# Kernel optimization log

Measured on AMD Instinct MI355X. Metric: run time of the kernel, lower is better.

## Reference

```python
import jax, jax.numpy as jnp
from jax import lax
import numpy as np

T, I, H, H2 = 2048, 64, 256, 1024  # time steps, input feats, hidden, hidden2


def _lstm(x, Wih, Whh, bih, bhh):
    """PyTorch-convention LSTM. x: [T, B, I]; Wih: [4H, I]; Whh: [4H, H].
    Gate order i, f, g, o. Returns hidden states [T, B, H]."""
    Hd = Whh.shape[1]
    b = bih + bhh
    xw = jnp.einsum('tbi,gi->tbg', x, Wih) + b  # precompute input projections

    def step(carry, xt):
        h, c = carry
        z = xt + h @ Whh.T
        i, f, g, o = jnp.split(z, 4, axis=-1)
        c = jax.nn.sigmoid(f) * c + jax.nn.sigmoid(i) * jnp.tanh(g)
        h = jax.nn.sigmoid(o) * jnp.tanh(c)
        return (h, c), h

    h0 = jnp.zeros((x.shape[1], Hd), x.dtype)
    _, hs = lax.scan(step, (h0, h0), xw)
    return hs


def setup_inputs() -> dict:
    key = jax.random.key(0)
    ks = jax.random.split(key, 16)
    s1 = 1.0 / np.sqrt(H)
    s2 = 1.0 / np.sqrt(H2)
    d = {
        'x': jax.random.normal(ks[0], (T, I, 21), jnp.float32),
        'Wih1': jax.random.uniform(ks[1], (4 * H, I), jnp.float32, -s1, s1),
        'Whh1': jax.random.uniform(ks[2], (4 * H, H), jnp.float32, -s1, s1),
        'bih1': jax.random.uniform(ks[3], (4 * H,), jnp.float32, -s1, s1),
        'bhh1': jax.random.uniform(ks[4], (4 * H,), jnp.float32, -s1, s1),
        'Wih2': jax.random.uniform(ks[5], (4 * H2, H * 21), jnp.float32, -s2, s2),
        'Whh2': jax.random.uniform(ks[6], (4 * H2, H2), jnp.float32, -s2, s2),
        'bih2': jax.random.uniform(ks[7], (4 * H2,), jnp.float32, -s2, s2),
        'bhh2': jax.random.uniform(ks[8], (4 * H2,), jnp.float32, -s2, s2),
        'Wih3': jax.random.uniform(ks[9], (4 * H, H2), jnp.float32, -s1, s1),
        'Whh3': jax.random.uniform(ks[10], (4 * H, H), jnp.float32, -s1, s1),
        'bih3': jax.random.uniform(ks[11], (4 * H,), jnp.float32, -s1, s1),
        'bhh3': jax.random.uniform(ks[12], (4 * H,), jnp.float32, -s1, s1),
        'Wfc': jax.random.uniform(ks[13], (21, H), jnp.float32, -s1, s1),
        'bfc': jax.random.uniform(ks[14], (21,), jnp.float32, -s1, s1),
    }
    return d


def reference(x, Wih1, Whh1, bih1, bhh1, Wih2, Whh2, bih2, bhh2,
              Wih3, Whh3, bih3, bhh3, Wfc, bfc):
    # The 21-iteration torch loop runs lstm1 independently on each of the 21
    # channel slices with batch=1; fold the 21 channels into the batch dim.
    x1 = jnp.transpose(x, (0, 2, 1))           # [T, 21, I]
    h1 = _lstm(x1, Wih1, Whh1, bih1, bhh1)     # [T, 21, H]
    # x_torch[:, :, i*H:(i+1)*H] = channel i -> channel-major concat
    xcat = h1.reshape(T, 1, 21 * H)            # [T, 1, 21H]
    h2 = _lstm(xcat, Wih2, Whh2, bih2, bhh2)   # [T, 1, H2]
    h3 = _lstm(h2, Wih3, Whh3, bih3, bhh3)     # [T, 1, H]
    out = h3 @ Wfc.T + bfc                     # [T, 1, 21]
    return out
```

## Files before the change

### kernel.cpp

```cpp
#include <hip/hip_runtime.h>


#define T_STEPS 2048
#define SENT 0xFFFFFFFFu

using f4v   = __attribute__((ext_vector_type(4))) float;
using s8v   = __attribute__((ext_vector_type(8))) short;
using u16x8 = __attribute__((ext_vector_type(8))) unsigned short;
using u32x4 = __attribute__((ext_vector_type(4))) unsigned;

__device__ __forceinline__ unsigned short f2bf(float v) {
  unsigned u = __float_as_uint(v);
  u = (u + 0x7FFFu + ((u >> 16) & 1u)) >> 16;
  return (unsigned short)u;
}
__device__ __forceinline__ float bf2f(unsigned short b) {
  return __uint_as_float(((unsigned)b) << 16);
}
__device__ __forceinline__ unsigned packhl(float v) {
  unsigned short hb = f2bf(v);
  unsigned short lb = f2bf(v - bf2f(hb));
  return (((unsigned)hb) << 16) | lb;
}
__device__ __forceinline__ float unpackhl(unsigned p) {
  return __uint_as_float(p & 0xFFFF0000u) + __uint_as_float(p << 16);
}
__device__ __forceinline__ float sigm(float x) { return 1.0f / (1.0f + __expf(-x)); }
__device__ __forceinline__ float tanh_f(float x) {
  float ax = fabsf(x);
  float e = __expf(-2.0f * ax);
  float t = (1.0f - e) / (1.0f + e);
  return copysignf(t, x);
}
__device__ __forceinline__ unsigned ld_agent32(const unsigned* p) {
  return __hip_atomic_load(p, __ATOMIC_RELAXED, __HIP_MEMORY_SCOPE_AGENT);
}
__device__ __forceinline__ void st_agent32(unsigned* p, unsigned v) {
  __hip_atomic_store(p, v, __ATOMIC_RELAXED, __HIP_MEMORY_SCOPE_AGENT);
}
__device__ __forceinline__ void ctr_add(unsigned* p) {
  __hip_atomic_fetch_add(p, 1u, __ATOMIC_RELAXED, __HIP_MEMORY_SCOPE_AGENT);
}
__device__ __forceinline__ void poll_ctr(const unsigned* p, unsigned tgt) {
  unsigned n = 0;
  while (ld_agent32(p) < tgt) {
    if (++n > (1u << 22)) break;
    __builtin_amdgcn_s_sleep(4);
  }
}
__device__ __forceinline__ u32x4 ld16_coh(const unsigned* addr) {
  u32x4 c;
  asm volatile("global_load_dwordx4 %0, %1, off sc0 sc1\n\t"
               "s_waitcnt vmcnt(0)"
               : "=&v"(c) : "v"(addr) : "memory");
  return c;
}
#define VMCNT0() asm volatile("s_waitcnt vmcnt(0)" ::: "memory")

#define L16(M) M(0) M(1) M(2) M(3) M(4) M(5) M(6) M(7) M(8) M(9) M(10) M(11) \
  M(12) M(13) M(14) M(15)
#define L64(M) L16(M) M(16) M(17) M(18) M(19) M(20) M(21) M(22) M(23) M(24) \
  M(25) M(26) M(27) M(28) M(29) M(30) M(31) M(32) M(33) M(34) M(35) M(36) \
  M(37) M(38) M(39) M(40) M(41) M(42) M(43) M(44) M(45) M(46) M(47) M(48) \
  M(49) M(50) M(51) M(52) M(53) M(54) M(55) M(56) M(57) M(58) M(59) M(60) \
  M(61) M(62) M(63)

__device__ __forceinline__ void unpack8(u32x4 a, u32x4 b, u16x8& hi, u16x8& lo) {
#pragma unroll
  for (int j = 0; j < 4; ++j) {
    hi[j]     = (unsigned short)(a[j] >> 16);
    lo[j]     = (unsigned short)(a[j] & 0xFFFFu);
    hi[4 + j] = (unsigned short)(b[j] >> 16);
    lo[4 + j] = (unsigned short)(b[j] & 0xFFFFu);
  }
}

__device__ void gemm_tile_packed(
    const unsigned* __restrict__ Ap, const unsigned short* __restrict__ Bh,
    const unsigned short* __restrict__ Bl, const float* __restrict__ b1,
    const float* __restrict__ b2, unsigned* __restrict__ C,
    int tm, int tn, int K, int N, char* smem)
{
  unsigned short* lds = (unsigned short*)smem;
  const size_t m0 = (size_t)tm * 128, n0 = (size_t)tn * 128;
  const int tid = threadIdx.x, lane = tid & 63, w = tid >> 6;
  const int wr = w >> 1, wc = w & 1;
  const int srow = tid >> 2, sc8 = (tid & 3) * 8;

  const unsigned* pA = Ap + m0 * K;
  const unsigned short* pBh = Bh + n0 * K;
  const unsigned short* pBl = Bl + n0 * K;

  f4v acc[4][4];
#pragma unroll
  for (int i = 0; i < 4; ++i)
#pragma unroll
    for (int j = 0; j < 4; ++j) acc[i][j] = f4v{0.f, 0.f, 0.f, 0.f};

  u32x4 a00, a01, a10, a11;
  u16x8 s4, s5, s6, s7;
#define LOADK(k0)                                                           \
  a00 = *(const u32x4*)(pA + (size_t)srow * K + (k0) + sc8);                \
  a01 = *(const u32x4*)(pA + (size_t)srow * K + (k0) + sc8 + 4);            \
  a10 = *(const u32x4*)(pA + (size_t)(srow + 64) * K + (k0) + sc8);         \
  a11 = *(const u32x4*)(pA + (size_t)(srow + 64) * K + (k0) + sc8 + 4);     \
  s4 = *(const u16x8*)(pBh + (size_t)srow * K + (k0) + sc8);                \
  s5 = *(const u16x8*)(pBh + (size_t)(srow + 64) * K + (k0) + sc8);         \
  s6 = *(const u16x8*)(pBl + (size_t)srow * K + (k0) + sc8);                \
  s7 = *(const u16x8*)(pBl + (size_t)(srow + 64) * K + (k0) + sc8);

  LOADK(0);
  const int fr = lane & 15, fko = (lane >> 4) * 8;
  for (int k0 = 0; k0 < K; k0 += 32) {
    u16x8 h0, l0, h1, l1;
    unpack8(a00, a01, h0, l0);
    unpack8(a10, a11, h1, l1);
    *(u16x8*)&lds[0     +  srow       * 32 + sc8] = h0;
    *(u16x8*)&lds[0     + (srow + 64) * 32 + sc8] = h1;
    *(u16x8*)&lds[4096  +  srow       * 32 + sc8] = l0;
    *(u16x8*)&lds[4096  + (srow + 64) * 32 + sc8] = l1;
    *(u16x8*)&lds[8192  +  srow       * 32 + sc8] = s4;
    *(u16x8*)&lds[8192  + (srow + 64) * 32 + sc8] = s5;
    *(u16x8*)&lds[12288 +  srow       * 32 + sc8] = s6;
    *(u16x8*)&lds[12288 + (srow + 64) * 32 + sc8] = s7;
    __syncthreads();
    if (k0 + 32 < K) { LOADK(k0 + 32); }
    s8v afh[4], afl[4], bfh[4], bfl[4];
#pragma unroll
    for (int i = 0; i < 4; ++i) {
      int ar = (64 * wr + 16 * i + fr) * 32 + fko;
      int br = (64 * wc + 16 * i + fr) * 32 + fko;
      afh[i] = *(const s8v*)&lds[0 + ar];
      afl[i] = *(const s8v*)&lds[4096 + ar];
      bfh[i] = *(const s8v*)&lds[8192 + br];
      bfl[i] = *(const s8v*)&lds[12288 + br];
    }
#pragma unroll
    for (int mi = 0; mi < 4; ++mi)
#pragma unroll
      for (int ni = 0; ni < 4; ++ni) {
        acc[mi][ni] = __builtin_amdgcn_mfma_f32_16x16x32_bf16(afh[mi], bfh[ni], acc[mi][ni], 0, 0, 0);
        acc[mi][ni] = __builtin_amdgcn_mfma_f32_16x16x32_bf16(afh[mi], bfl[ni], acc[mi][ni], 0, 0, 0);
        acc[mi][ni] = __builtin_amdgcn_mfma_f32_16x16x32_bf16(afl[mi], bfh[ni], acc[mi][ni], 0, 0, 0);
      }
    __syncthreads();
  }
#undef LOADK
  const int er = (lane >> 4) * 4, ec = lane & 15;
#pragma unroll
  for (int ni = 0; ni < 4; ++ni) {
    size_t col = n0 + 64 * wc + 16 * ni + ec;
    float bv = b1[col] + b2[col];
#pragma unroll
    for (int mi = 0; mi < 4; ++mi) {
      size_t row = m0 + 64 * wr + 16 * mi + er;
#pragma unroll
      for (int rr = 0; rr < 4; ++rr)
        st_agent32(&C[(row + rr) * N + col], __float_as_uint(acc[mi][ni][rr] + bv));
    }
  }
}

__global__ __launch_bounds__(256, 1) void mega_kernel(
    const float* __restrict__ x,
    const float* __restrict__ Wih1, const float* __restrict__ Whh1,
    const float* __restrict__ bih1, const float* __restrict__ bhh1,
    const float* __restrict__ Whh2,
    const float* __restrict__ bih2, const float* __restrict__ bhh2,
    const float* __restrict__ Whh3,
    const float* __restrict__ bih3, const float* __restrict__ bhh3,
    unsigned* __restrict__ h1r0, unsigned* __restrict__ h2r0,
    unsigned* __restrict__ h3r0, unsigned* __restrict__ cnt,
    unsigned* __restrict__ h1rows, unsigned* __restrict__ h2rows,
    unsigned* __restrict__ h3rows,
    float* __restrict__ xw2, float* __restrict__ xw3,
    const unsigned short* __restrict__ wih2h, const unsigned short* __restrict__ wih2l,
    const unsigned short* __restrict__ wih3h, const unsigned short* __restrict__ wih3l)
{
  __shared__ __align__(16) char smem[32768];
  unsigned* ready1 = cnt + 0;
  unsigned* done2  = cnt + 16;
  unsigned* ready2 = cnt + 32;
  unsigned* done3  = cnt + 48;
  const int wg = blockIdx.x;
  const int widx = threadIdx.x >> 6, lane = threadIdx.x & 63;

  if (wg < 84) {
    const int c = wg / 4, sub = wg % 4;
    const int gwv = sub * 4 + widx;
    const int u16i = lane & 15, g = lane >> 4;
    const int grow = g * 256 + gwv * 16 + u16i;

    const f4v* wsrc = (const f4v*)(Whh1 + (size_t)grow * 256);
    const f4v* xsrc = (const f4v*)(Wih1 + (size_t)grow * 64);
#define DH(i) f4v m##i = wsrc[i];
#define DX(i) f4v n##i = xsrc[i];
    L64(DH)
    L16(DX)
#undef DH
#undef DX
    const float bias = bih1[grow] + bhh1[grow];

    float* const hb = (float*)smem + widx * 320;
    float* const xq = hb + 256;

    float cst = 0.0f;
    float xpre = x[(size_t)lane * 21 + c];

    for (int t = 0; t < T_STEPS; ++t) {
      xq[lane] = xpre;
      if (t + 1 < T_STEPS) xpre = x[(size_t)(t + 1) * 1344 + lane * 21 + c];
      const unsigned* src = t ? h1rows + (size_t)(t - 1) * 5376 + c * 256
                              : h1r0 + c * 256;
      const unsigned* addr = src + 4 * lane;
      u32x4 c0;
      unsigned n = 0;
      for (;;) {
        c0 = ld16_coh(addr);
        bool ok = (c0[0] != SENT) && (c0[1] != SENT) &&
                  (c0[2] != SENT) && (c0[3] != SENT);
        if (ok || ++n > (1u << 18)) break;
      }
      *(f4v*)&hb[4 * lane] = f4v{unpackhl(c0[0]), unpackhl(c0[1]),
                                 unpackhl(c0[2]), unpackhl(c0[3])};
      float a0 = 0, a1 = 0, a2 = 0, a3 = 0;
#define FH(i) { f4v h4 = *(const f4v*)&hb[4 * i]; \
  a0 = fmaf(m##i[0], h4[0], a0); a1 = fmaf(m##i[1], h4[1], a1); \
  a2 = fmaf(m##i[2], h4[2], a2); a3 = fmaf(m##i[3], h4[3], a3); }
#define FX(i) { f4v x4 = *(const f4v*)&xq[4 * i]; \
  a0 = fmaf(n##i[0], x4[0], a0); a1 = fmaf(n##i[1], x4[1], a1); \
  a2 = fmaf(n##i[2], x4[2], a2); a3 = fmaf(n##i[3], x4[3], a3); }
      L64(FH)
      L16(FX)
#undef FH
#undef FX
      float z = (a0 + a1) + (a2 + a3) + bias;
      float zi = __shfl(z, u16i);
      float zf = __shfl(z, 16 + u16i);
      float zg = __shfl(z, 32 + u16i);
      float zo = __shfl(z, 48 + u16i);
      if (lane < 16) {
        float cn = sigm(zf) * cst + sigm(zi) * tanh_f(zg);
        float hn = sigm(zo) * tanh_f(cn);
        cst = cn;
        st_agent32(&h1rows[(size_t)t * 5376 + c * 256 + gwv * 16 + lane], packhl(hn));
      }
      if ((t & 127) == 127) {
        VMCNT0();
        if (lane == 0) ctr_add(&ready1[t >> 7]);
      }
    }
  } else if (wg < 148) {
    const int gw = (wg - 84) * 4 + widx;
    const int q = lane >> 4, r4 = lane & 15;
    const int u = r4 & 3, g = r4 >> 2;
    const int grow = g * 1024 + gw * 4 + u;

    const f4v* wsrc = (const f4v*)(Whh2 + (size_t)grow * 1024 + q * 256);
#define DW(i) f4v w##i = wsrc[i];
    L64(DW)
#undef DW

    float* const wls = (float*)smem + widx * 1040;
    const float* const qreg = wls + q * 260;

    float cst = 0.0f;
    float xwn = 0.0f;

    for (int t = 0; t < T_STEPS; ++t) {
      float xwv;
      if ((t & 127) == 0) {
        poll_ctr(&done2[t >> 7], 32);
        xwv = xw2[(size_t)t * 4096 + grow];
      } else xwv = xwn;
      {
        const unsigned* src = t ? h2rows + (size_t)(t - 1) * 1024 : h2r0;
        const unsigned* addr = src + 4 * lane;
        u32x4 c0, c1, c2, c3;
        unsigned n = 0;
        for (;;) {
          asm volatile(
              "global_load_dwordx4 %0, %4, off sc0 sc1\n\t"
              "global_load_dwordx4 %1, %4, off offset:1024 sc0 sc1\n\t"
              "global_load_dwordx4 %2, %4, off offset:2048 sc0 sc1\n\t"
              "global_load_dwordx4 %3, %4, off offset:3072 sc0 sc1\n\t"
              "s_waitcnt vmcnt(0)"
              : "=&v"(c0), "=&v"(c1), "=&v"(c2), "=&v"(c3)
              : "v"(addr) : "memory");
          bool ok = true;
#pragma unroll
          for (int j = 0; j < 4; ++j)
            ok = ok && (c0[j] != SENT) && (c1[j] != SENT) &&
                       (c2[j] != SENT) && (c3[j] != SENT);
          if (ok || ++n > (1u << 18)) break;
        }
        *(f4v*)&wls[0 * 260 + 4 * lane] = f4v{unpackhl(c0[0]), unpackhl(c0[1]), unpackhl(c0[2]), unpackhl(c0[3])};
        *(f4v*)&wls[1 * 260 + 4 * lane] = f4v{unpackhl(c1[0]), unpackhl(c1[1]), unpackhl(c1[2]), unpackhl(c1[3])};
        *(f4v*)&wls[2 * 260 + 4 * lane] = f4v{unpackhl(c2[0]), unpackhl(c2[1]), unpackhl(c2[2]), unpackhl(c2[3])};
        *(f4v*)&wls[3 * 260 + 4 * lane] = f4v{unpackhl(c3[0]), unpackhl(c3[1]), unpackhl(c3[2]), unpackhl(c3[3])};
      }
      float a0 = 0, a1 = 0, a2 = 0, a3 = 0;
#define FW(i) { f4v h4 = *(const f4v*)&qreg[4 * i]; \
  a0 = fmaf(w##i[0], h4[0], a0); a1 = fmaf(w##i[1], h4[1], a1); \
  a2 = fmaf(w##i[2], h4[2], a2); a3 = fmaf(w##i[3], h4[3], a3); }
      L64(FW)
#undef FW
      float z = (a0 + a1) + (a2 + a3);
      z += __shfl_xor(z, 16);
      z += __shfl_xor(z, 32);
      z += xwv;
      float zi  = __shfl(z, u);
      float zf  = __shfl(z, 4 + u);
      float zg2 = __shfl(z, 8 + u);
      float zo  = __shfl(z, 12 + u);
      if (lane < 4) {
        float cn = sigm(zf) * cst + sigm(zi) * tanh_f(zg2);
        float hn = sigm(zo) * tanh_f(cn);
        cst = cn;
        st_agent32(&h2rows[(size_t)t * 1024 + gw * 4 + lane], packhl(hn));
      }
      if ((t & 127) == 127) {
        VMCNT0();
        if (lane == 0) ctr_add(&ready2[t >> 7]);
      }
      if (t + 1 < T_STEPS && ((t + 1) & 127) != 0)
        xwn = xw2[(size_t)(t + 1) * 4096 + grow];
    }
  } else if (wg < 152) {
    const int gw = (wg - 148) * 4 + widx;
    const int u16i = lane & 15, g = lane >> 4;
    const int grow = g * 256 + gw * 16 + u16i;

    const f4v* wsrc = (const f4v*)(Whh3 + (size_t)grow * 256);
#define DW(i) f4v w##i = wsrc[i];
    L64(DW)
#undef DW

    float* const hb = (float*)smem + widx * 256;
    float cst = 0.0f;
    float xwn = 0.0f;

    for (int t = 0; t < T_STEPS; ++t) {
      float xwv;
      if ((t & 127) == 0) {
        poll_ctr(&done3[t >> 7], 8);
        xwv = xw3[(size_t)t * 1024 + grow];
      } else xwv = xwn;
      const unsigned* src = t ? h3rows + (size_t)(t - 1) * 256 : h3r0;
      const unsigned* addr = src + 4 * lane;
      u32x4 c0;
      unsigned n = 0;
      for (;;) {
        c0 = ld16_coh(addr);
        bool ok = (c0[0] != SENT) && (c0[1] != SENT) &&
                  (c0[2] != SENT) && (c0[3] != SENT);
        if (ok || ++n > (1u << 18)) break;
      }
      *(f4v*)&hb[4 * lane] = f4v{__uint_as_float(c0[0]), __uint_as_float(c0[1]),
                                 __uint_as_float(c0[2]), __uint_as_float(c0[3])};
      float a0 = 0, a1 = 0, a2 = 0, a3 = 0;
#define FW(i) { f4v h4 = *(const f4v*)&hb[4 * i]; \
  a0 = fmaf(w##i[0], h4[0], a0); a1 = fmaf(w##i[1], h4[1], a1); \
  a2 = fmaf(w##i[2], h4[2], a2); a3 = fmaf(w##i[3], h4[3], a3); }
      L64(FW)
#undef FW
      float z = (a0 + a1) + (a2 + a3) + xwv;
      float zi = __shfl(z, u16i);
      float zf = __shfl(z, 16 + u16i);
      float zg = __shfl(z, 32 + u16i);
      float zo = __shfl(z, 48 + u16i);
      if (lane < 16) {
        float cn = sigm(zf) * cst + sigm(zi) * tanh_f(zg);
        float hn = sigm(zo) * tanh_f(cn);
        cst = cn;
        st_agent32(&h3rows[(size_t)t * 256 + gw * 16 + lane], __float_as_uint(hn));
      }
      if (t + 1 < T_STEPS && ((t + 1) & 127) != 0)
        xwn = xw3[(size_t)(t + 1) * 1024 + grow];
    }
  } else if (wg < 206) {
    const int pw = wg - 152;
    for (int i = pw; i < 512; i += 54) {
      int tm = i >> 5, tn = i & 31;
      poll_ctr(&ready1[tm], 336);
      gemm_tile_packed(h1rows, wih2h, wih2l, bih2, bhh2,
                       (unsigned*)xw2, tm, tn, 5376, 4096, smem);
      VMCNT0();
      __syncthreads();
      if (threadIdx.x == 0) ctr_add(&done2[tm]);
      __syncthreads();
    }
  } else {
    const int pw = wg - 206;
    for (int i = pw; i < 128; i += 14) {
      int tm = i >> 3, tn = i & 7;
      poll_ctr(&ready2[tm], 256);
      gemm_tile_packed(h2rows, wih3h, wih3l, bih3, bhh3,
                       (unsigned*)xw3, tm, tn, 1024, 1024, smem);
      VMCNT0();
      __syncthreads();
      if (threadIdx.x == 0) ctr_add(&done3[tm]);
      __syncthreads();
    }
  }
}

__global__ void split_kernel(const float* __restrict__ src,
                             unsigned short* __restrict__ hi,
                             unsigned short* __restrict__ lo, int n) {
  int i = blockIdx.x * 256 + threadIdx.x;
  if (i < n) {
    float v = src[i];
    unsigned short hb = f2bf(v);
    hi[i] = hb;
    lo[i] = f2bf(v - bf2f(hb));
  }
}

__global__ void fc_kernel(const float* __restrict__ h3, const float* __restrict__ Wfc,
                          const float* __restrict__ bfc, float* __restrict__ out) {
  int t = blockIdx.x, m = threadIdx.x;
  if (m < 21) {
    const float* hp = h3 + (size_t)t * 256;
    const float* wp = Wfc + m * 256;
    float a = 0.0f;
#pragma unroll 8
    for (int j = 0; j < 256; ++j) a = fmaf(wp[j], hp[j], a);
    out[t * 21 + m] = a + bfc[m];
  }
}

extern "C" void kernel_launch(void* const* d_in, const int* in_sizes, int n_in,
                              void* d_out, int out_size, void* d_ws, size_t ws_size,
                              hipStream_t stream) {
  const float* x    = (const float*)d_in[0];
  const float* Wih1 = (const float*)d_in[1];
  const float* Whh1 = (const float*)d_in[2];
  const float* bih1 = (const float*)d_in[3];
  const float* bhh1 = (const float*)d_in[4];
  const float* Wih2 = (const float*)d_in[5];
  const float* Whh2 = (const float*)d_in[6];
  const float* bih2 = (const float*)d_in[7];
  const float* bhh2 = (const float*)d_in[8];
  const float* Wih3 = (const float*)d_in[9];
  const float* Whh3 = (const float*)d_in[10];
  const float* bih3 = (const float*)d_in[11];
  const float* bhh3 = (const float*)d_in[12];
  const float* Wfc  = (const float*)d_in[13];
  const float* bfc  = (const float*)d_in[14];
  float* out = (float*)d_out;

  const size_t WS_NEEDED = 188776448;
  if (ws_size < WS_NEEDED) return;
  char* ws = (char*)d_ws;
  unsigned* h1r0 = (unsigned*)(ws + 0);
  unsigned* h2r0 = (unsigned*)(ws + 21504);
  unsigned* h3r0 = (unsigned*)(ws + 25600);
  unsigned* cnt  = (unsigned*)(ws + 26624);
  unsigned* h1rows = (unsigned*)(ws + 32768);
  unsigned* h2rows = (unsigned*)(ws + 44072960);
  unsigned* h3rows = (unsigned*)(ws + 52461568);
  float* xw2 = (float*)(ws + 54558720);
  float* xw3 = (float*)(ws + 88113152);
  unsigned short* wih2h = (unsigned short*)(ws + 96501760);
  unsigned short* wih2l = (unsigned short*)(ws + 140541952);
  unsigned short* wih3h = (unsigned short*)(ws + 184582144);
  unsigned short* wih3l = (unsigned short*)(ws + 186679296);

  hipMemsetAsync(ws, 0, 32768, stream);
  hipMemsetAsync(ws + 32768, 0xFF, 54525952, stream);

  const int nW2 = 4096 * 5376;
  split_kernel<<<(nW2 + 255) / 256, 256, 0, stream>>>(Wih2, wih2h, wih2l, nW2);
  const int nW3 = 1024 * 1024;
  split_kernel<<<(nW3 + 255) / 256, 256, 0, stream>>>(Wih3, wih3h, wih3l, nW3);

  mega_kernel<<<220, 256, 0, stream>>>(
      x, Wih1, Whh1, bih1, bhh1,
      Whh2, bih2, bhh2, Whh3, bih3, bhh3,
      h1r0, h2r0, h3r0, cnt,
      h1rows, h2rows, h3rows, xw2, xw3,
      wih2h, wih2l, wih3h, wih3l);

  fc_kernel<<<2048, 64, 0, stream>>>((const float*)h3rows, Wfc, bfc, out);
}
```

Measured before the change: 9.738 ms.

## Spread LSTM2 recurrence over twice the waves with 8-lane K-split

Moves the layer-2 recurrent step from 64 to 128 workgroups. Each wave now owns 2 hidden units instead of 4, holds half as many Whh2 registers, and splits K eight ways with an xor-shuffle reduction. This shortens the per-step serial dot-product chain on the critical recurrence. In exchange there are fewer GEMM producer workgroups for xw2 and xw3, a larger grid of 252 blocks that must all be co-resident for the spin-wait scheme, and more waves polling h2. The GEMM tile loads also switch to nontemporal loads.

```diff
diff --git a/kernel.cpp b/kernel.cpp
--- a/kernel.cpp
+++ b/kernel.cpp
@@ -57,10 +57,24 @@
 }
 #define VMCNT0() asm volatile("s_waitcnt vmcnt(0)" ::: "memory")
 
+#define ISSUE4(r0, r1, r2, r3, ad)                                          \
+  asm volatile(                                                             \
+      "global_load_dwordx4 %0, %4, off sc0 sc1\n\t"                         \
+      "global_load_dwordx4 %1, %4, off offset:1024 sc0 sc1\n\t"             \
+      "global_load_dwordx4 %2, %4, off offset:2048 sc0 sc1\n\t"             \
+      "global_load_dwordx4 %3, %4, off offset:3072 sc0 sc1"                 \
+      : "=&v"(r0), "=&v"(r1), "=&v"(r2), "=&v"(r3) : "v"(ad) : "memory")
+#define OK4(r0, r1, r2, r3)                                                 \
+  ((r0[0] != SENT) && (r0[1] != SENT) && (r0[2] != SENT) && (r0[3] != SENT) && \
+   (r1[0] != SENT) && (r1[1] != SENT) && (r1[2] != SENT) && (r1[3] != SENT) && \
+   (r2[0] != SENT) && (r2[1] != SENT) && (r2[2] != SENT) && (r2[3] != SENT) && \
+   (r3[0] != SENT) && (r3[1] != SENT) && (r3[2] != SENT) && (r3[3] != SENT))
+
 #define L16(M) M(0) M(1) M(2) M(3) M(4) M(5) M(6) M(7) M(8) M(9) M(10) M(11) \
   M(12) M(13) M(14) M(15)
-#define L64(M) L16(M) M(16) M(17) M(18) M(19) M(20) M(21) M(22) M(23) M(24) \
-  M(25) M(26) M(27) M(28) M(29) M(30) M(31) M(32) M(33) M(34) M(35) M(36) \
+#define L32(M) L16(M) M(16) M(17) M(18) M(19) M(20) M(21) M(22) M(23) M(24) \
+  M(25) M(26) M(27) M(28) M(29) M(30) M(31)
+#define L64(M) L32(M) M(32) M(33) M(34) M(35) M(36) \
   M(37) M(38) M(39) M(40) M(41) M(42) M(43) M(44) M(45) M(46) M(47) M(48) \
   M(49) M(50) M(51) M(52) M(53) M(54) M(55) M(56) M(57) M(58) M(59) M(60) \
   M(61) M(62) M(63)
@@ -99,15 +113,15 @@
 
   u32x4 a00, a01, a10, a11;
   u16x8 s4, s5, s6, s7;
-#define LOADK(k0)                                                           \
-  a00 = *(const u32x4*)(pA + (size_t)srow * K + (k0) + sc8);                \
-  a01 = *(const u32x4*)(pA + (size_t)srow * K + (k0) + sc8 + 4);            \
-  a10 = *(const u32x4*)(pA + (size_t)(srow + 64) * K + (k0) + sc8);         \
-  a11 = *(const u32x4*)(pA + (size_t)(srow + 64) * K + (k0) + sc8 + 4);     \
-  s4 = *(const u16x8*)(pBh + (size_t)srow * K + (k0) + sc8);                \
-  s5 = *(const u16x8*)(pBh + (size_t)(srow + 64) * K + (k0) + sc8);         \
-  s6 = *(const u16x8*)(pBl + (size_t)srow * K + (k0) + sc8);                \
-  s7 = *(const u16x8*)(pBl + (size_t)(srow + 64) * K + (k0) + sc8);
+#define LOADK(k0)                                                                    \
+  a00 = __builtin_nontemporal_load((const u32x4*)(pA + (size_t)srow * K + (k0) + sc8));        \
+  a01 = __builtin_nontemporal_load((const u32x4*)(pA + (size_t)srow * K + (k0) + sc8 + 4));    \
+  a10 = __builtin_nontemporal_load((const u32x4*)(pA + (size_t)(srow + 64) * K + (k0) + sc8)); \
+  a11 = __builtin_nontemporal_load((const u32x4*)(pA + (size_t)(srow + 64) * K + (k0) + sc8 + 4)); \
+  s4 = __builtin_nontemporal_load((const u16x8*)(pBh + (size_t)srow * K + (k0) + sc8));        \
+  s5 = __builtin_nontemporal_load((const u16x8*)(pBh + (size_t)(srow + 64) * K + (k0) + sc8)); \
+  s6 = __builtin_nontemporal_load((const u16x8*)(pBl + (size_t)srow * K + (k0) + sc8));        \
+  s7 = __builtin_nontemporal_load((const u16x8*)(pBl + (size_t)(srow + 64) * K + (k0) + sc8));
 
   LOADK(0);
   const int fr = lane & 15, fko = (lane >> 4) * 8;
@@ -250,84 +264,92 @@
         if (lane == 0) ctr_add(&ready1[t >> 7]);
       }
     }
-  } else if (wg < 148) {
+  } else if (wg < 212) {
     const int gw = (wg - 84) * 4 + widx;
-    const int q = lane >> 4, r4 = lane & 15;
-    const int u = r4 & 3, g = r4 >> 2;
-    const int grow = g * 1024 + gw * 4 + u;
-
-    const f4v* wsrc = (const f4v*)(Whh2 + (size_t)grow * 1024 + q * 256);
+    const int r8 = lane >> 3, e = lane & 7;
+    const int g = r8 >> 1, u = r8 & 1;
+    const int grow = g * 1024 + 2 * gw + u;
+
+    const f4v* wsrc = (const f4v*)(Whh2 + (size_t)grow * 1024 + e * 128);
 #define DW(i) f4v w##i = wsrc[i];
-    L64(DW)
+    L32(DW)
 #undef DW
-
-    float* const wls = (float*)smem + widx * 1040;
-    const float* const qreg = wls + q * 260;
+    asm volatile("" : "+v"(w0), "+v"(w1), "+v"(w2), "+v"(w3),
+                      "+v"(w4), "+v"(w5), "+v"(w6), "+v"(w7));
+    asm volatile("" : "+v"(w8), "+v"(w9), "+v"(w10), "+v"(w11),
+                      "+v"(w12), "+v"(w13), "+v"(w14), "+v"(w15));
+    asm volatile("" : "+v"(w16), "+v"(w17), "+v"(w18), "+v"(w19),
+                      "+v"(w20), "+v"(w21), "+v"(w22), "+v"(w23));
+    asm volatile("" : "+v"(w24), "+v"(w25), "+v"(w26), "+v"(w27),
+                      "+v"(w28), "+v"(w29), "+v"(w30), "+v"(w31));
+
+    float* const hls = (float*)smem + widx * 1060;
+    const float* const eb = hls + e * 132;
+    const int sb = (lane >> 5) * 132 + 4 * (lane & 31);
+    const int ug = lane & 1;
 
     float cst = 0.0f;
-    float xwn = 0.0f;
+    float xwi = 0, xwf = 0, xwg = 0, xwo = 0;
+    if (lane < 2) {
+      xwi = xw2[0 * 4096 + 0 * 1024 + 2 * gw + lane];
+    }
 
     for (int t = 0; t < T_STEPS; ++t) {
-      float xwv;
       if ((t & 127) == 0) {
         poll_ctr(&done2[t >> 7], 32);
-        xwv = xw2[(size_t)t * 4096 + grow];
-      } else xwv = xwn;
+        if (lane < 2) {
+          const float* xp = xw2 + (size_t)t * 4096 + 2 * gw + lane;
+          xwi = xp[0]; xwf = xp[1024]; xwg = xp[2048]; xwo = xp[3072];
+        }
+      }
       {
         const unsigned* src = t ? h2rows + (size_t)(t - 1) * 1024 : h2r0;
         const unsigned* addr = src + 4 * lane;
         u32x4 c0, c1, c2, c3;
         unsigned n = 0;
         for (;;) {
-          asm volatile(
-              "global_load_dwordx4 %0, %4, off sc0 sc1\n\t"
-              "global_load_dwordx4 %1, %4, off offset:1024 sc0 sc1\n\t"
-              "global_load_dwordx4 %2, %4, off offset:2048 sc0 sc1\n\t"
-              "global_load_dwordx4 %3, %4, off offset:3072 sc0 sc1\n\t"
-              "s_waitcnt vmcnt(0)"
-              : "=&v"(c0), "=&v"(c1), "=&v"(c2), "=&v"(c3)
-              : "v"(addr) : "memory");
-          bool ok = true;
-#pragma unroll
-          for (int j = 0; j < 4; ++j)
-            ok = ok && (c0[j] != SENT) && (c1[j] != SENT) &&
-                       (c2[j] != SENT) && (c3[j] != SENT);
-          if (ok || ++n > (1u << 18)) break;
+          ISSUE4(c0, c1, c2, c3, addr);
+          asm volatile("s_waitcnt vmcnt(0)"
+                       : "+v"(c0), "+v"(c1), "+v"(c2), "+v"(c3) :: "memory");
+          if (OK4(c0, c1, c2, c3) || ++n > (1u << 18)) break;
         }
-        *(f4v*)&wls[0 * 260 + 4 * lane] = f4v{unpackhl(c0[0]), unpackhl(c0[1]), unpackhl(c0[2]), unpackhl(c0[3])};
-        *(f4v*)&wls[1 * 260 + 4 * lane] = f4v{unpackhl(c1[0]), unpackhl(c1[1]), unpackhl(c1[2]), unpackhl(c1[3])};
-        *(f4v*)&wls[2 * 260 + 4 * lane] = f4v{unpackhl(c2[0]), unpackhl(c2[1]), unpackhl(c2[2]), unpackhl(c2[3])};
-        *(f4v*)&wls[3 * 260 + 4 * lane] = f4v{unpackhl(c3[0]), unpackhl(c3[1]), unpackhl(c3[2]), unpackhl(c3[3])};
+        *(f4v*)&hls[sb]       = f4v{unpackhl(c0[0]), unpackhl(c0[1]), unpackhl(c0[2]), unpackhl(c0[3])};
+        *(f4v*)&hls[sb + 264] = f4v{unpackhl(c1[0]), unpackhl(c1[1]), unpackhl(c1[2]), unpackhl(c1[3])};
+        *(f4v*)&hls[sb + 528] = f4v{unpackhl(c2[0]), unpackhl(c2[1]), unpackhl(c2[2]), unpackhl(c2[3])};
+        *(f4v*)&hls[sb + 792] = f4v{unpackhl(c3[0]), unpackhl(c3[1]), unpackhl(c3[2]), unpackhl(c3[3])};
       }
       float a0 = 0, a1 = 0, a2 = 0, a3 = 0;
-#define FW(i) { f4v h4 = *(const f4v*)&qreg[4 * i]; \
+#define FW(i) { f4v h4 = *(const f4v*)&eb[4 * i]; \
   a0 = fmaf(w##i[0], h4[0], a0); a1 = fmaf(w##i[1], h4[1], a1); \
   a2 = fmaf(w##i[2], h4[2], a2); a3 = fmaf(w##i[3], h4[3], a3); }
-      L64(FW)
+      L32(FW)
 #undef FW
       float z = (a0 + a1) + (a2 + a3);
-      z += __shfl_xor(z, 16);
-      z += __shfl_xor(z, 32);
-      z += xwv;
-      float zi  = __shfl(z, u);
-      float zf  = __shfl(z, 4 + u);
-      float zg2 = __shfl(z, 8 + u);
-      float zo  = __shfl(z, 12 + u);
-      if (lane < 4) {
-        float cn = sigm(zf) * cst + sigm(zi) * tanh_f(zg2);
-        float hn = sigm(zo) * tanh_f(cn);
+      z += __shfl_xor(z, 1);
+      z += __shfl_xor(z, 2);
+      z += __shfl_xor(z, 4);
+      float zi = __shfl(z, (0 + ug) * 8);
+      float zf = __shfl(z, (2 + ug) * 8);
+      float zg2 = __shfl(z, (4 + ug) * 8);
+      float zo = __shfl(z, (6 + ug) * 8);
+      if (lane < 2) {
+        float vi = zi + xwi, vf = zf + xwf, vg = zg2 + xwg, vo = zo + xwo;
+        float cn = sigm(vf) * cst + sigm(vi) * tanh_f(vg);
+        float hn = sigm(vo) * tanh_f(cn);
         cst = cn;
-        st_agent32(&h2rows[(size_t)t * 1024 + gw * 4 + lane], packhl(hn));
+        st_agent32(&h2rows[(size_t)t * 1024 + 2 * gw + lane], packhl(hn));
       }
       if ((t & 127) == 127) {
         VMCNT0();
         if (lane == 0) ctr_add(&ready2[t >> 7]);
       }
-      if (t + 1 < T_STEPS && ((t + 1) & 127) != 0)
-        xwn = xw2[(size_t)(t + 1) * 4096 + grow];
-    }
-  } else if (wg < 152) {
-    const int gw = (wg - 148) * 4 + widx;
+      if (lane < 2 && t + 1 < T_STEPS && ((t + 1) & 127) != 0) {
+        const float* xp = xw2 + (size_t)(t + 1) * 4096 + 2 * gw + lane;
+        xwi = xp[0]; xwf = xp[1024]; xwg = xp[2048]; xwo = xp[3072];
+      }
+    }
+  } else if (wg < 216) {
+    const int gw = (wg - 212) * 4 + widx;
     const int u16i = lane & 15, g = lane >> 4;
     const int grow = g * 256 + gw * 16 + u16i;
 
@@ -378,9 +400,9 @@
       if (t + 1 < T_STEPS && ((t + 1) & 127) != 0)
         xwn = xw3[(size_t)(t + 1) * 1024 + grow];
     }
-  } else if (wg < 206) {
-    const int pw = wg - 152;
-    for (int i = pw; i < 512; i += 54) {
+  } else if (wg < 244) {
+    const int pw = wg - 216;
+    for (int i = pw; i < 512; i += 28) {
       int tm = i >> 5, tn = i & 31;
       poll_ctr(&ready1[tm], 336);
       gemm_tile_packed(h1rows, wih2h, wih2l, bih2, bhh2,
@@ -391,10 +413,10 @@
       __syncthreads();
     }
   } else {
-    const int pw = wg - 206;
-    for (int i = pw; i < 128; i += 14) {
+    const int pw = wg - 244;
+    for (int i = pw; i < 128; i += 8) {
       int tm = i >> 3, tn = i & 7;
-      poll_ctr(&ready2[tm], 256);
+      poll_ctr(&ready2[tm], 512);
       gemm_tile_packed(h2rows, wih3h, wih3l, bih3, bhh3,
                        (unsigned*)xw3, tm, tn, 1024, 1024, smem);
       VMCNT0();
@@ -475,7 +497,7 @@
   const int nW3 = 1024 * 1024;
   split_kernel<<<(nW3 + 255) / 256, 256, 0, stream>>>(Wih3, wih3h, wih3l, nW3);
 
-  mega_kernel<<<220, 256, 0, stream>>>(
+  mega_kernel<<<252, 256, 0, stream>>>(
       x, Wih1, Whh1, bih1, bhh1,
       Whh2, bih2, bhh2, Whh3, bih3, bhh3,
       h1r0, h2r0, h3r0, cnt,
```

Measured after the change: 10.71 ms. 10.0% more time.
